# Performance work log

Measured on AMD Instinct MI355X. Metric: run time of the kernel, lower is better.

## Reference

```python
import jax, jax.numpy as jnp
import numpy as np

N_A = 100000
N_B = 100000


def _mean_agg(x_src, src, dst, n_dst):
    # gather source features along edges, mean-aggregate into destination nodes
    msgs = x_src[src]                                        # [E, d]
    s = jax.ops.segment_sum(msgs, dst, num_segments=n_dst)   # [n_dst, d]
    ones = jnp.ones((dst.shape[0], 1), dtype=x_src.dtype)
    cnt = jax.ops.segment_sum(ones, dst, num_segments=n_dst)
    return s / jnp.maximum(cnt, jnp.asarray(1.0, x_src.dtype))


def setup_inputs() -> dict:
    key = jax.random.key(0)
    ks = jax.random.split(key, 13)
    E = 1200000
    d = 64
    return {
        "x_A": jax.random.normal(ks[0], (N_A, d), jnp.float32),
        "x_B": jax.random.normal(ks[1], (N_B, d), jnp.float32),
        "Wn": jax.random.normal(ks[2], (2, 3, d, d), jnp.float32) * 0.1,
        "Wr": jax.random.normal(ks[3], (2, 3, d, d), jnp.float32) * 0.1,
        "b": jax.random.normal(ks[4], (2, 3, d), jnp.float32) * 0.1,
        "W_out": jax.random.normal(ks[5], (d, d), jnp.float32) * 0.1,
        "b_out": jax.random.normal(ks[6], (d,), jnp.float32) * 0.1,
        "src0": jax.random.randint(ks[7], (E,), 0, N_A, jnp.int64 if jax.config.jax_enable_x64 else jnp.int32),
        "dst0": jax.random.randint(ks[8], (E,), 0, N_B, jnp.int32),
        "src1": jax.random.randint(ks[9], (E,), 0, N_B, jnp.int32),
        "dst1": jax.random.randint(ks[10], (E,), 0, N_A, jnp.int32),
        "src2": jax.random.randint(ks[11], (E,), 0, N_A, jnp.int32),
        "dst2": jax.random.randint(ks[12], (E,), 0, N_A, jnp.int32),
    }


def reference(x_A, x_B, Wn, Wr, b, W_out, b_out,
              src0, dst0, src1, dst1, src2, dst2):
    # Two stacked heterogeneous conv layers (SAGEConv-style per edge type,
    # summed across edge types per destination node type), then Linear+ReLU head.
    for l in range(2):
        m0 = _mean_agg(x_A, src0, dst0, N_B)  # A -> B
        m1 = _mean_agg(x_B, src1, dst1, N_A)  # B -> A
        m2 = _mean_agg(x_A, src2, dst2, N_A)  # A -> A
        new_B = m0 @ Wn[l, 0] + x_B @ Wr[l, 0] + b[l, 0]
        new_A = (m1 @ Wn[l, 1] + x_A @ Wr[l, 1] + b[l, 1]
                 + m2 @ Wn[l, 2] + x_A @ Wr[l, 2] + b[l, 2])
        x_A, x_B = new_A, new_B
    out_A = jax.nn.relu(x_A @ W_out + b_out)
    out_B = jax.nn.relu(x_B @ W_out + b_out)
    return jnp.concatenate([out_A, out_B], axis=0)  # [N_A + N_B, d]
```

## Files before the change

### kernel.cpp

```cpp
#include <hip/hip_runtime.h>
#include <hip/hip_bf16.h>

typedef __bf16 bf16_t;
typedef unsigned short u16;
typedef short short8 __attribute__((ext_vector_type(8)));
typedef float f32x4 __attribute__((ext_vector_type(4)));

#define BSHIFT 9
#define CAP 8192
#define TILE 16384

__device__ inline short f2bs(float v) {
    bf16_t h = (bf16_t)v;
    return __builtin_bit_cast(short, h);
}
__device__ inline float uif(unsigned u) { return __builtin_bit_cast(float, u); }

__global__ __launch_bounds__(256) void prep_convert(
    const float* __restrict__ xA, const float* __restrict__ xB,
    const float* __restrict__ Wn, const float* __restrict__ Wr,
    const float* __restrict__ Wout, const float* __restrict__ b,
    const float* __restrict__ b_out,
    u16* __restrict__ plane0, u16* __restrict__ wh,
    int* __restrict__ gcursor, float* __restrict__ biasC,
    int NA, int NB, int K) {
    int nA4 = NA * 16, nB4 = NB * 16;
    int bA = (nA4 + 255) / 256, bB = (nB4 + 255) / 256;
    int bi = blockIdx.x;
    int tid = threadIdx.x;
    if (bi < bA + bB) {
        const float* in = (bi < bA) ? xA : xB;
        u16* out = (bi < bA) ? plane0 : plane0 + (size_t)NA * 64;
        int i = (bi < bA ? bi : bi - bA) * 256 + tid;
        int n4 = (bi < bA) ? nA4 : nB4;
        if (i >= n4) return;
        float4 v = ((const float4*)in)[i];
        u16 o[4];
        o[0] = (u16)f2bs(v.x); o[1] = (u16)f2bs(v.y);
        o[2] = (u16)f2bs(v.z); o[3] = (u16)f2bs(v.w);
        *(uint2*)(out + (size_t)i * 4) = *(uint2*)o;
        return;
    }
    if (bi < bA + bB + 11) {
        int mat = bi - bA - bB;
        u16* dstp = wh + (size_t)mat * 4096;
        for (int i = tid; i < 4096; i += 256) {
            int k = i >> 6, n = i & 63;
            float v;
            if (mat < 6) v = Wn[(size_t)mat * 4096 + i];
            else if (mat < 8) v = Wr[(size_t)((mat - 6) * 3 + 0) * 4096 + i];
            else if (mat < 10) v = Wr[(size_t)((mat - 8) * 3 + 1) * 4096 + i]
                                 + Wr[(size_t)((mat - 8) * 3 + 2) * 4096 + i];
            else v = Wout[i];
            dstp[n * 64 + k] = (u16)f2bs(v);
        }
        return;
    }
    if (bi < bA + bB + 11 + 5) {
        int c = bi - bA - bB - 11;
        const float* Wsrc;
        const float* Wsrc2 = nullptr;
        if (c == 0) Wsrc = Wn + (size_t)3 * 4096;
        else if (c == 1) Wsrc = Wr + (size_t)3 * 4096;
        else if (c == 2) Wsrc = Wn + (size_t)4 * 4096;
        else if (c == 3) Wsrc = Wn + (size_t)5 * 4096;
        else { Wsrc = Wr + (size_t)4 * 4096; Wsrc2 = Wr + (size_t)5 * 4096; }
        __shared__ float Ws[64 * 64];
        __shared__ float Wo[64 * 64];
        for (int i = tid; i < 4096; i += 256) {
            float w = Wsrc[i];
            if (Wsrc2) w += Wsrc2[i];
            Ws[i] = w;
            Wo[i] = Wout[i];
        }
        __syncthreads();
        u16* dstp = wh + (size_t)(11 + c) * 4096;
        for (int it = 0; it < 16; ++it) {
            int i = it * 256 + tid;
            int k = i >> 6, n = i & 63;
            float s0 = 0.f, s1 = 0.f, s2 = 0.f, s3 = 0.f;
#pragma unroll
            for (int j = 0; j < 64; j += 4) {
                s0 += Ws[k * 64 + j]     * Wo[j * 64 + n];
                s1 += Ws[k * 64 + j + 1] * Wo[(j + 1) * 64 + n];
                s2 += Ws[k * 64 + j + 2] * Wo[(j + 2) * 64 + n];
                s3 += Ws[k * 64 + j + 3] * Wo[(j + 3) * 64 + n];
            }
            dstp[n * 64 + k] = (u16)f2bs((s0 + s1) + (s2 + s3));
        }
        return;
    }
    for (int i = tid; i < K; i += 256) gcursor[i] = i * CAP;
    if (tid < 64) {
        int n = tid;
        float s0 = b_out[n], s1 = b_out[n];
        for (int j = 0; j < 64; j++) {
            float wo = Wout[j * 64 + n];
            s0 += b[3 * 64 + j] * wo;
            s1 += (b[4 * 64 + j] + b[5 * 64 + j]) * wo;
        }
        biasC[0 * 64 + n] = b[0 * 64 + n];
        biasC[1 * 64 + n] = b[1 * 64 + n] + b[2 * 64 + n];
        biasC[2 * 64 + n] = s0;
        biasC[3 * 64 + n] = s1;
    }
}

__global__ __launch_bounds__(1024) void partition_kernel(
    const int* __restrict__ s0, const int* __restrict__ d0,
    const int* __restrict__ s1, const int* __restrict__ d1,
    const int* __restrict__ s2, const int* __restrict__ d2,
    int* __restrict__ gcursor, int* __restrict__ pairs,
    int NB, int NA, int E, int total) {
    __shared__ int hist[1024];
    __shared__ int gbase[1024];
    int tid = threadIdx.x;
    for (int tile = blockIdx.x * TILE; tile < total; tile += gridDim.x * TILE) {
        hist[tid] = 0;
        __syncthreads();
        int mybkt[16], mypk[16], myrank[16];
#pragma unroll
        for (int j = 0; j < 16; j++) {
            int idx = tile + j * 1024 + tid;
            int g = -1, s = 0;
            if (idx < total) {
                if (idx < E) { s = s0[idx]; g = d0[idx]; }
                else if (idx < 2 * E) { s = s1[idx - E]; g = NB + d1[idx - E]; }
                else { s = s2[idx - 2 * E]; g = NB + NA + d2[idx - 2 * E]; }
            }
            if (g >= 0) {
                mybkt[j] = g >> BSHIFT;
                mypk[j] = ((g & ((1 << BSHIFT) - 1)) << 17) | s;
                myrank[j] = atomicAdd(&hist[mybkt[j]], 1);
            } else mybkt[j] = -1;
        }
        __syncthreads();
        {
            int c = hist[tid];
            if (c) gbase[tid] = atomicAdd(&gcursor[tid], c);
        }
        __syncthreads();
#pragma unroll
        for (int j = 0; j < 16; j++) {
            if (mybkt[j] >= 0)
                pairs[gbase[mybkt[j]] + myrank[j]] = mypk[j];
        }
        __syncthreads();
    }
}

__global__ __launch_bounds__(512) void bucket_fill(const int* __restrict__ pairs,
                                                   const int* __restrict__ gcursor,
                                                   int* __restrict__ off_s,
                                                   int* __restrict__ off_e,
                                                   int* __restrict__ colidx, int M) {
    int b = blockIdx.x;
    int gb = b << BSHIFT;
    __shared__ int cnt[512], cur[512], wsum[8];
    int tid = threadIdx.x;
    int lane = tid & 63, w = tid >> 6;
    int p0 = b * CAP, p1 = gcursor[b];
    cnt[tid] = 0;
    __syncthreads();
    for (int e = p0 + tid; e < p1; e += 512)
        atomicAdd(&cnt[(unsigned)pairs[e] >> 17], 1);
    __syncthreads();
    int v = cnt[tid];
    int x = v;
#pragma unroll
    for (int off = 1; off < 64; off <<= 1) {
        int n = __shfl_up(x, off);
        if (lane >= off) x += n;
    }
    if (lane == 63) wsum[w] = x;
    __syncthreads();
    if (tid == 0) {
        int s = 0;
#pragma unroll
        for (int i = 0; i < 8; i++) { int t = wsum[i]; wsum[i] = s; s += t; }
    }
    __syncthreads();
    int excl = x - v + wsum[w];
    cur[tid] = excl;
    int g = gb + tid;
    if (g < M) { off_s[g] = p0 + excl; off_e[g] = p0 + excl + v; }
    __syncthreads();
    for (int e = p0 + tid; e < p1; e += 512) {
        int p = pairs[e];
        int pos = atomicAdd(&cur[(unsigned)p >> 17], 1);
        colidx[p0 + pos] = p & 0x1FFFF;
    }
}

__device__ __forceinline__ void acc8(uint4 u, f32x4& a0, f32x4& a1) {
    a0[0] += uif(u.x << 16); a0[1] += uif(u.x & 0xFFFF0000u);
    a0[2] += uif(u.y << 16); a0[3] += uif(u.y & 0xFFFF0000u);
    a1[0] += uif(u.z << 16); a1[1] += uif(u.z & 0xFFFF0000u);
    a1[2] += uif(u.w << 16); a1[3] += uif(u.w & 0xFFFF0000u);
}

__global__ __launch_bounds__(256) void gather_all(const u16* __restrict__ plane,
                                                  const int* __restrict__ colidx,
                                                  const int* __restrict__ off_s,
                                                  const int* __restrict__ off_e,
                                                  u16* __restrict__ meanB,
                                                  u16* __restrict__ meanA1,
                                                  u16* __restrict__ meanA2,
                                                  int NB, int NA) {
    int wid = (blockIdx.x * 256 + threadIdx.x) >> 6;
    int lane = threadIdx.x & 63;
    int oct = lane >> 3, fl = lane & 7;
    int M = NB + 2 * NA;
    int grow = wid * 8 + oct;
    if (grow >= M) return;

    const char* tab;
    u16* outp;
    int orow;
    if (grow < NB) { tab = (const char*)plane; outp = meanB; orow = grow; }
    else if (grow < NB + NA) { tab = (const char*)(plane + (size_t)NA * 64); outp = meanA1; orow = grow - NB; }
    else { tab = (const char*)plane; outp = meanA2; orow = grow - NB - NA; }

    int s0 = off_s[grow], s1 = off_e[grow];
    unsigned fo = (unsigned)(fl << 4);
    f32x4 a0 = {0.f, 0.f, 0.f, 0.f}, a1 = {0.f, 0.f, 0.f, 0.f};

    int e = s0;
    if (e + 3 < s1) {
        int c0 = colidx[e], c1 = colidx[e + 1];
        int c2 = colidx[e + 2], c3 = colidx[e + 3];
        while (e + 7 < s1) {
            uint4 u0 = *(const uint4*)(tab + (((unsigned)c0 << 7) | fo));
            uint4 u1 = *(const uint4*)(tab + (((unsigned)c1 << 7) | fo));
            uint4 u2 = *(const uint4*)(tab + (((unsigned)c2 << 7) | fo));
            uint4 u3 = *(const uint4*)(tab + (((unsigned)c3 << 7) | fo));
            c0 = colidx[e + 4]; c1 = colidx[e + 5];
            c2 = colidx[e + 6]; c3 = colidx[e + 7];
            acc8(u0, a0, a1); acc8(u1, a0, a1);
            acc8(u2, a0, a1); acc8(u3, a0, a1);
            e += 4;
        }
        {
            uint4 u0 = *(const uint4*)(tab + (((unsigned)c0 << 7) | fo));
            uint4 u1 = *(const uint4*)(tab + (((unsigned)c1 << 7) | fo));
            uint4 u2 = *(const uint4*)(tab + (((unsigned)c2 << 7) | fo));
            uint4 u3 = *(const uint4*)(tab + (((unsigned)c3 << 7) | fo));
            acc8(u0, a0, a1); acc8(u1, a0, a1);
            acc8(u2, a0, a1); acc8(u3, a0, a1);
            e += 4;
        }
    }
    for (; e < s1; ++e) {
        int c = colidx[e];
        uint4 u = *(const uint4*)(tab + (((unsigned)c << 7) | fo));
        acc8(u, a0, a1);
    }

    float inv = 1.0f / fmaxf((float)(s1 - s0), 1.0f);
    u16 o[8];
#pragma unroll
    for (int i = 0; i < 4; i++) o[i] = (u16)f2bs(a0[i] * inv);
#pragma unroll
    for (int i = 0; i < 4; i++) o[4 + i] = (u16)f2bs(a1[i] * inv);
    *(uint4*)(outp + (size_t)orow * 64 + fl * 8) = *(uint4*)o;
}

template <int NM, int RELU, int OUTF32>
__device__ __forceinline__ void lin_body(
    const u16* __restrict__ m0, const u16* __restrict__ m1,
    const u16* __restrict__ x,
    const u16* __restrict__ Wm0t, const u16* __restrict__ Wm1t,
    const u16* __restrict__ Wxt,
    const float* __restrict__ bias64,
    void* __restrict__ outv, int nrows, int blk) {
    const int lane = threadIdx.x & 63;
    const int wave = threadIdx.x >> 6;
    const int row0 = blk * 64 + wave * 16;
    if (row0 >= nrows) return;
    const int r = lane & 15;
    const int q = lane >> 4;

    f32x4 acc[4];
#pragma unroll
    for (int t = 0; t < 4; t++) {
        float bv = bias64[t * 16 + r];
        acc[t][0] = bv; acc[t][1] = bv; acc[t][2] = bv; acc[t][3] = bv;
    }

    const int arow = row0 + r;
    const bool avalid = arow < nrows;
    short8 zf;
#pragma unroll
    for (int j = 0; j < 8; j++) zf[j] = 0;

#pragma unroll
    for (int ks = 0; ks < 2; ks++) {
        short8 af = avalid ? *(const short8*)(m0 + (size_t)arow * 64 + ks * 32 + q * 8) : zf;
        short8 xf = avalid ? *(const short8*)(x + (size_t)arow * 64 + ks * 32 + q * 8) : zf;
        short8 bf_;
        if (NM >= 2) bf_ = avalid ? *(const short8*)(m1 + (size_t)arow * 64 + ks * 32 + q * 8) : zf;
#pragma unroll
        for (int t = 0; t < 4; t++) {
            size_t widx = (size_t)(t * 16 + r) * 64 + ks * 32 + q * 8;
            acc[t] = __builtin_amdgcn_mfma_f32_16x16x32_bf16(af, *(const short8*)(Wm0t + widx), acc[t], 0, 0, 0);
            if (NM >= 2)
                acc[t] = __builtin_amdgcn_mfma_f32_16x16x32_bf16(bf_, *(const short8*)(Wm1t + widx), acc[t], 0, 0, 0);
            acc[t] = __builtin_amdgcn_mfma_f32_16x16x32_bf16(xf, *(const short8*)(Wxt + widx), acc[t], 0, 0, 0);
        }
    }

#pragma unroll
    for (int t = 0; t < 4; t++) {
#pragma unroll
        for (int rr = 0; rr < 4; rr++) {
            int row = row0 + q * 4 + rr;
            if (row < nrows) {
                float v = acc[t][rr];
                if (RELU) v = fmaxf(v, 0.0f);
                if (OUTF32)
                    __builtin_nontemporal_store(v, (float*)outv + (size_t)row * 64 + t * 16 + r);
                else
                    ((u16*)outv)[(size_t)row * 64 + t * 16 + r] = (u16)f2bs(v);
            }
        }
    }
}

__global__ __launch_bounds__(256) void layer1_kernel(
    const u16* __restrict__ plane_in, u16* __restrict__ plane_out,
    const u16* __restrict__ meanB, const u16* __restrict__ meanA1,
    const u16* __restrict__ meanA2, const u16* __restrict__ wh,
    const float* __restrict__ biasC, int NA, int NB, int blocksB) {
    if ((int)blockIdx.x < blocksB) {
        lin_body<1, 0, 0>(meanB, nullptr, plane_in + (size_t)NA * 64,
                          wh + (size_t)0 * 4096, nullptr, wh + (size_t)6 * 4096,
                          biasC + 0 * 64,
                          plane_out + (size_t)NA * 64, NB, blockIdx.x);
    } else {
        lin_body<2, 0, 0>(meanA1, meanA2, plane_in,
                          wh + (size_t)1 * 4096, wh + (size_t)2 * 4096, wh + (size_t)8 * 4096,
                          biasC + 1 * 64,
                          plane_out, NA, blockIdx.x - blocksB);
    }
}

__global__ __launch_bounds__(256) void layer2_head_kernel(
    const u16* __restrict__ plane_in,
    const u16* __restrict__ meanB, const u16* __restrict__ meanA1,
    const u16* __restrict__ meanA2, const u16* __restrict__ wh,
    const float* __restrict__ biasC,
    float* __restrict__ out, int NA, int NB, int blocksB) {
    if ((int)blockIdx.x < blocksB) {
        lin_body<1, 1, 1>(meanB, nullptr, plane_in + (size_t)NA * 64,
                          wh + (size_t)11 * 4096, nullptr, wh + (size_t)12 * 4096,
                          biasC + 2 * 64,
                          out + (size_t)NA * 64, NB, blockIdx.x);
    } else {
        lin_body<2, 1, 1>(meanA1, meanA2, plane_in,
                          wh + (size_t)13 * 4096, wh + (size_t)14 * 4096, wh + (size_t)15 * 4096,
                          biasC + 3 * 64,
                          out, NA, blockIdx.x - blocksB);
    }
}

extern "C" void kernel_launch(void* const* d_in, const int* in_sizes, int n_in,
                              void* d_out, int out_size, void* d_ws, size_t ws_size,
                              hipStream_t stream) {
    const float* xA_in = (const float*)d_in[0];
    const float* xB_in = (const float*)d_in[1];
    const float* Wn = (const float*)d_in[2];
    const float* Wr = (const float*)d_in[3];
    const float* b = (const float*)d_in[4];
    const float* W_out = (const float*)d_in[5];
    const float* b_out = (const float*)d_in[6];
    const int* src0 = (const int*)d_in[7];
    const int* dst0 = (const int*)d_in[8];
    const int* src1 = (const int*)d_in[9];
    const int* dst1 = (const int*)d_in[10];
    const int* src2 = (const int*)d_in[11];
    const int* dst2 = (const int*)d_in[12];

    const int NA = in_sizes[0] / 64;
    const int NB = in_sizes[1] / 64;
    const int E = in_sizes[7];
    const int M = NB + NA + NA;
    const int total = 3 * E;
    const int K = (M + (1 << BSHIFT) - 1) >> BSHIFT;

    const size_t PL = (size_t)(NA + NB) * 64;
    u16* plane[2];
    plane[0] = (u16*)d_ws;
    plane[1] = plane[0] + PL;
    u16* wh     = plane[1] + PL;
    u16* meanB  = wh + 16 * 4096;
    u16* meanA1 = meanB + (size_t)NB * 64;
    u16* meanA2 = meanA1 + (size_t)NA * 64;
    int* gcursor= (int*)(meanA2 + (size_t)NA * 64);
    float* biasC= (float*)(gcursor + 1024);
    int* off_s  = (int*)(biasC + 256);
    int* off_e  = off_s + M;
    int* colidx = off_e + M;
    int* pairs  = (int*)meanB;

    int bA = (NA * 16 + 255) / 256, bB = (NB * 16 + 255) / 256;
    prep_convert<<<bA + bB + 11 + 5 + 1, 256, 0, stream>>>(
        xA_in, xB_in, Wn, Wr, W_out, b, b_out,
        plane[0], wh, gcursor, biasC, NA, NB, K);

    int ntiles = (total + TILE - 1) / TILE;
    partition_kernel<<<ntiles, 1024, 0, stream>>>(src0, dst0, src1, dst1, src2, dst2,
                                                  gcursor, pairs, NB, NA, E, total);
    bucket_fill<<<K, 512, 0, stream>>>(pairs, gcursor, off_s, off_e, colidx, M);

    const int blocksB = (NB + 63) / 64;
    const int blocksA = (NA + 63) / 64;
    gather_all<<<(M + 31) / 32, 256, 0, stream>>>(plane[0], colidx, off_s, off_e,
                                                  meanB, meanA1, meanA2, NB, NA);
    layer1_kernel<<<blocksB + blocksA, 256, 0, stream>>>(
        plane[0], plane[1], meanB, meanA1, meanA2, wh, biasC, NA, NB, blocksB);

    gather_all<<<(M + 31) / 32, 256, 0, stream>>>(plane[1], colidx, off_s, off_e,
                                                  meanB, meanA1, meanA2, NB, NA);
    layer2_head_kernel<<<blocksB + blocksA, 256, 0, stream>>>(
        plane[1], meanB, meanA1, meanA2, wh, biasC, (float*)d_out, NA, NB, blocksB);
}
```

Before: 411.0 us.

## Fuse neighbor mean-gather with MFMA linear layer through shared memory

Replaces the separate gather_all and per-layer linear kernels with one fused kernel per layer. Each block gathers mean-aggregated neighbor rows into an LDS tile and immediately applies the MFMA projections, so the bf16 mean buffers are no longer written to and re-read from global memory. This removes two launches and the intermediate traffic. In exchange, blocks are smaller (32 or 16 rows), so more blocks are launched and weight fragments are reloaded per block, and the pairs scratch buffer is moved to sit after colidx.

```diff
diff --git a/kernel.cpp b/kernel.cpp
--- a/kernel.cpp
+++ b/kernel.cpp
@@ -199,32 +199,10 @@
     a1[2] += uif(u.w << 16); a1[3] += uif(u.w & 0xFFFF0000u);
 }
 
-__global__ __launch_bounds__(256) void gather_all(const u16* __restrict__ plane,
-                                                  const int* __restrict__ colidx,
-                                                  const int* __restrict__ off_s,
-                                                  const int* __restrict__ off_e,
-                                                  u16* __restrict__ meanB,
-                                                  u16* __restrict__ meanA1,
-                                                  u16* __restrict__ meanA2,
-                                                  int NB, int NA) {
-    int wid = (blockIdx.x * 256 + threadIdx.x) >> 6;
-    int lane = threadIdx.x & 63;
-    int oct = lane >> 3, fl = lane & 7;
-    int M = NB + 2 * NA;
-    int grow = wid * 8 + oct;
-    if (grow >= M) return;
-
-    const char* tab;
-    u16* outp;
-    int orow;
-    if (grow < NB) { tab = (const char*)plane; outp = meanB; orow = grow; }
-    else if (grow < NB + NA) { tab = (const char*)(plane + (size_t)NA * 64); outp = meanA1; orow = grow - NB; }
-    else { tab = (const char*)plane; outp = meanA2; orow = grow - NB - NA; }
-
-    int s0 = off_s[grow], s1 = off_e[grow];
-    unsigned fo = (unsigned)(fl << 4);
+__device__ __forceinline__ uint4 gather_seg(const char* __restrict__ tab,
+                                            const int* __restrict__ colidx,
+                                            int s0, int s1, unsigned fo) {
     f32x4 a0 = {0.f, 0.f, 0.f, 0.f}, a1 = {0.f, 0.f, 0.f, 0.f};
-
     int e = s0;
     if (e + 3 < s1) {
         int c0 = colidx[e], c1 = colidx[e + 1];
@@ -255,111 +233,133 @@
         uint4 u = *(const uint4*)(tab + (((unsigned)c << 7) | fo));
         acc8(u, a0, a1);
     }
-
     float inv = 1.0f / fmaxf((float)(s1 - s0), 1.0f);
     u16 o[8];
 #pragma unroll
     for (int i = 0; i < 4; i++) o[i] = (u16)f2bs(a0[i] * inv);
 #pragma unroll
     for (int i = 0; i < 4; i++) o[4 + i] = (u16)f2bs(a1[i] * inv);
-    *(uint4*)(outp + (size_t)orow * 64 + fl * 8) = *(uint4*)o;
-}
-
-template <int NM, int RELU, int OUTF32>
-__device__ __forceinline__ void lin_body(
-    const u16* __restrict__ m0, const u16* __restrict__ m1,
-    const u16* __restrict__ x,
-    const u16* __restrict__ Wm0t, const u16* __restrict__ Wm1t,
-    const u16* __restrict__ Wxt,
-    const float* __restrict__ bias64,
-    void* __restrict__ outv, int nrows, int blk) {
-    const int lane = threadIdx.x & 63;
-    const int wave = threadIdx.x >> 6;
-    const int row0 = blk * 64 + wave * 16;
-    if (row0 >= nrows) return;
-    const int r = lane & 15;
-    const int q = lane >> 4;
-
-    f32x4 acc[4];
-#pragma unroll
-    for (int t = 0; t < 4; t++) {
-        float bv = bias64[t * 16 + r];
-        acc[t][0] = bv; acc[t][1] = bv; acc[t][2] = bv; acc[t][3] = bv;
-    }
-
-    const int arow = row0 + r;
-    const bool avalid = arow < nrows;
+    return *(uint4*)o;
+}
+
+template <int L2>
+__global__ __launch_bounds__(256) void fused_layer(
+    const u16* __restrict__ plane_in, void* __restrict__ outv,
+    const int* __restrict__ colidx,
+    const int* __restrict__ off_s, const int* __restrict__ off_e,
+    const u16* __restrict__ wh, const float* __restrict__ biasC,
+    int NA, int NB, int blocksBf) {
+    __shared__ __align__(16) u16 mS[32][72];
+    const int tid = threadIdx.x;
+    const int w = tid >> 6, lane = tid & 63;
+    const int oct = lane >> 3, fl = lane & 7;
+    const unsigned fo = (unsigned)(fl << 4);
+    const char* pA = (const char*)plane_in;
+    const char* pB = (const char*)(plane_in + (size_t)NA * 64);
+    const int r = lane & 15, q = lane >> 4;
     short8 zf;
 #pragma unroll
     for (int j = 0; j < 8; j++) zf[j] = 0;
 
-#pragma unroll
-    for (int ks = 0; ks < 2; ks++) {
-        short8 af = avalid ? *(const short8*)(m0 + (size_t)arow * 64 + ks * 32 + q * 8) : zf;
-        short8 xf = avalid ? *(const short8*)(x + (size_t)arow * 64 + ks * 32 + q * 8) : zf;
-        short8 bf_;
-        if (NM >= 2) bf_ = avalid ? *(const short8*)(m1 + (size_t)arow * 64 + ks * 32 + q * 8) : zf;
-#pragma unroll
-        for (int t = 0; t < 4; t++) {
+    if ((int)blockIdx.x < blocksBf) {
+        const int row0 = blockIdx.x * 32;
+        {
+            int seg = w * 8 + oct;
+            int brow = row0 + seg;
+            int s0 = 0, s1 = 0;
+            if (brow < NB) { s0 = off_s[brow]; s1 = off_e[brow]; }
+            uint4 mv = gather_seg(pA, colidx, s0, s1, fo);
+            *(uint4*)&mS[seg][fl * 8] = mv;
+        }
+        __syncthreads();
+        const int rt = w >> 1;
+        const int tbase = (w & 1) * 2;
+        const int arow = row0 + rt * 16 + r;
+        const bool av = arow < NB;
+        const u16* WmT = wh + (size_t)(L2 ? 11 : 0) * 4096;
+        const u16* WxT = wh + (size_t)(L2 ? 12 : 6) * 4096;
+        const float* bb = biasC + (size_t)(L2 ? 2 : 0) * 64;
+        f32x4 acc[2];
+#pragma unroll
+        for (int t2 = 0; t2 < 2; t2++) {
+            float bv = bb[(tbase + t2) * 16 + r];
+            acc[t2][0] = bv; acc[t2][1] = bv; acc[t2][2] = bv; acc[t2][3] = bv;
+        }
+#pragma unroll
+        for (int ks = 0; ks < 2; ks++) {
+            short8 am = *(const short8*)&mS[rt * 16 + r][ks * 32 + q * 8];
+            short8 ax = av ? *(const short8*)(pB + (size_t)arow * 128 + ks * 64 + q * 16) : zf;
+#pragma unroll
+            for (int t2 = 0; t2 < 2; t2++) {
+                size_t widx = (size_t)((tbase + t2) * 16 + r) * 64 + ks * 32 + q * 8;
+                acc[t2] = __builtin_amdgcn_mfma_f32_16x16x32_bf16(am, *(const short8*)(WmT + widx), acc[t2], 0, 0, 0);
+                acc[t2] = __builtin_amdgcn_mfma_f32_16x16x32_bf16(ax, *(const short8*)(WxT + widx), acc[t2], 0, 0, 0);
+            }
+        }
+#pragma unroll
+        for (int t2 = 0; t2 < 2; t2++) {
+            int col = (tbase + t2) * 16 + r;
+#pragma unroll
+            for (int rr = 0; rr < 4; rr++) {
+                int row = row0 + rt * 16 + q * 4 + rr;
+                if (row < NB) {
+                    float v = acc[t2][rr];
+                    if (L2) __builtin_nontemporal_store(fmaxf(v, 0.0f),
+                                (float*)outv + (size_t)(NA + row) * 64 + col);
+                    else ((u16*)outv)[(size_t)(NA + row) * 64 + col] = (u16)f2bs(v);
+                }
+            }
+        }
+    } else {
+        const int row0 = ((int)blockIdx.x - blocksBf) * 16;
+        {
+            int seg = w * 8 + oct;
+            int rrow = row0 + (seg & 15);
+            bool m2 = seg >= 16;
+            int s0 = 0, s1 = 0;
+            if (rrow < NA) {
+                int g = m2 ? (NB + NA + rrow) : (NB + rrow);
+                s0 = off_s[g]; s1 = off_e[g];
+            }
+            uint4 mv = gather_seg(m2 ? pA : pB, colidx, s0, s1, fo);
+            *(uint4*)&mS[seg][fl * 8] = mv;
+        }
+        __syncthreads();
+        const int t = w;
+        const int arow = row0 + r;
+        const bool av = arow < NA;
+        const u16* Wm1T = wh + (size_t)(L2 ? 13 : 1) * 4096;
+        const u16* Wm2T = wh + (size_t)(L2 ? 14 : 2) * 4096;
+        const u16* WxT  = wh + (size_t)(L2 ? 15 : 8) * 4096;
+        const float* bb = biasC + (size_t)(L2 ? 3 : 1) * 64;
+        f32x4 acc;
+        {
+            float bv = bb[t * 16 + r];
+            acc[0] = bv; acc[1] = bv; acc[2] = bv; acc[3] = bv;
+        }
+#pragma unroll
+        for (int ks = 0; ks < 2; ks++) {
+            short8 am1 = *(const short8*)&mS[r][ks * 32 + q * 8];
+            short8 am2 = *(const short8*)&mS[16 + r][ks * 32 + q * 8];
+            short8 ax = av ? *(const short8*)(pA + (size_t)arow * 128 + ks * 64 + q * 16) : zf;
             size_t widx = (size_t)(t * 16 + r) * 64 + ks * 32 + q * 8;
-            acc[t] = __builtin_amdgcn_mfma_f32_16x16x32_bf16(af, *(const short8*)(Wm0t + widx), acc[t], 0, 0, 0);
-            if (NM >= 2)
-                acc[t] = __builtin_amdgcn_mfma_f32_16x16x32_bf16(bf_, *(const short8*)(Wm1t + widx), acc[t], 0, 0, 0);
-            acc[t] = __builtin_amdgcn_mfma_f32_16x16x32_bf16(xf, *(const short8*)(Wxt + widx), acc[t], 0, 0, 0);
-        }
-    }
-
-#pragma unroll
-    for (int t = 0; t < 4; t++) {
-#pragma unroll
-        for (int rr = 0; rr < 4; rr++) {
-            int row = row0 + q * 4 + rr;
-            if (row < nrows) {
-                float v = acc[t][rr];
-                if (RELU) v = fmaxf(v, 0.0f);
-                if (OUTF32)
-                    __builtin_nontemporal_store(v, (float*)outv + (size_t)row * 64 + t * 16 + r);
-                else
-                    ((u16*)outv)[(size_t)row * 64 + t * 16 + r] = (u16)f2bs(v);
-            }
-        }
-    }
-}
-
-__global__ __launch_bounds__(256) void layer1_kernel(
-    const u16* __restrict__ plane_in, u16* __restrict__ plane_out,
-    const u16* __restrict__ meanB, const u16* __restrict__ meanA1,
-    const u16* __restrict__ meanA2, const u16* __restrict__ wh,
-    const float* __restrict__ biasC, int NA, int NB, int blocksB) {
-    if ((int)blockIdx.x < blocksB) {
-        lin_body<1, 0, 0>(meanB, nullptr, plane_in + (size_t)NA * 64,
-                          wh + (size_t)0 * 4096, nullptr, wh + (size_t)6 * 4096,
-                          biasC + 0 * 64,
-                          plane_out + (size_t)NA * 64, NB, blockIdx.x);
-    } else {
-        lin_body<2, 0, 0>(meanA1, meanA2, plane_in,
-                          wh + (size_t)1 * 4096, wh + (size_t)2 * 4096, wh + (size_t)8 * 4096,
-                          biasC + 1 * 64,
-                          plane_out, NA, blockIdx.x - blocksB);
-    }
-}
-
-__global__ __launch_bounds__(256) void layer2_head_kernel(
-    const u16* __restrict__ plane_in,
-    const u16* __restrict__ meanB, const u16* __restrict__ meanA1,
-    const u16* __restrict__ meanA2, const u16* __restrict__ wh,
-    const float* __restrict__ biasC,
-    float* __restrict__ out, int NA, int NB, int blocksB) {
-    if ((int)blockIdx.x < blocksB) {
-        lin_body<1, 1, 1>(meanB, nullptr, plane_in + (size_t)NA * 64,
-                          wh + (size_t)11 * 4096, nullptr, wh + (size_t)12 * 4096,
-                          biasC + 2 * 64,
-                          out + (size_t)NA * 64, NB, blockIdx.x);
-    } else {
-        lin_body<2, 1, 1>(meanA1, meanA2, plane_in,
-                          wh + (size_t)13 * 4096, wh + (size_t)14 * 4096, wh + (size_t)15 * 4096,
-                          biasC + 3 * 64,
-                          out, NA, blockIdx.x - blocksB);
+            acc = __builtin_amdgcn_mfma_f32_16x16x32_bf16(am1, *(const short8*)(Wm1T + widx), acc, 0, 0, 0);
+            acc = __builtin_amdgcn_mfma_f32_16x16x32_bf16(am2, *(const short8*)(Wm2T + widx), acc, 0, 0, 0);
+            acc = __builtin_amdgcn_mfma_f32_16x16x32_bf16(ax, *(const short8*)(WxT + widx), acc, 0, 0, 0);
+        }
+        {
+            int col = t * 16 + r;
+#pragma unroll
+            for (int rr = 0; rr < 4; rr++) {
+                int row = row0 + q * 4 + rr;
+                if (row < NA) {
+                    float v = acc[rr];
+                    if (L2) __builtin_nontemporal_store(fmaxf(v, 0.0f),
+                                (float*)outv + (size_t)row * 64 + col);
+                    else ((u16*)outv)[(size_t)row * 64 + col] = (u16)f2bs(v);
+                }
+            }
+        }
     }
 }
 
@@ -392,15 +392,12 @@
     plane[0] = (u16*)d_ws;
     plane[1] = plane[0] + PL;
     u16* wh     = plane[1] + PL;
-    u16* meanB  = wh + 16 * 4096;
-    u16* meanA1 = meanB + (size_t)NB * 64;
-    u16* meanA2 = meanA1 + (size_t)NA * 64;
-    int* gcursor= (int*)(meanA2 + (size_t)NA * 64);
+    int* gcursor= (int*)(wh + 16 * 4096);
     float* biasC= (float*)(gcursor + 1024);
     int* off_s  = (int*)(biasC + 256);
     int* off_e  = off_s + M;
     int* colidx = off_e + M;
-    int* pairs  = (int*)meanB;
+    int* pairs  = colidx + (size_t)K * CAP;
 
     int bA = (NA * 16 + 255) / 256, bB = (NB * 16 + 255) / 256;
     prep_convert<<<bA + bB + 11 + 5 + 1, 256, 0, stream>>>(
@@ -412,15 +409,10 @@
                                                   gcursor, pairs, NB, NA, E, total);
     bucket_fill<<<K, 512, 0, stream>>>(pairs, gcursor, off_s, off_e, colidx, M);
 
-    const int blocksB = (NB + 63) / 64;
-    const int blocksA = (NA + 63) / 64;
-    gather_all<<<(M + 31) / 32, 256, 0, stream>>>(plane[0], colidx, off_s, off_e,
-                                                  meanB, meanA1, meanA2, NB, NA);
-    layer1_kernel<<<blocksB + blocksA, 256, 0, stream>>>(
-        plane[0], plane[1], meanB, meanA1, meanA2, wh, biasC, NA, NB, blocksB);
-
-    gather_all<<<(M + 31) / 32, 256, 0, stream>>>(plane[1], colidx, off_s, off_e,
-                                                  meanB, meanA1, meanA2, NB, NA);
-    layer2_head_kernel<<<blocksB + blocksA, 256, 0, stream>>>(
-        plane[1], meanB, meanA1, meanA2, wh, biasC, (float*)d_out, NA, NB, blocksB);
-}
+    const int blocksBf = (NB + 31) / 32;
+    const int blocksAf = (NA + 15) / 16;
+    fused_layer<0><<<blocksBf + blocksAf, 256, 0, stream>>>(
+        plane[0], plane[1], colidx, off_s, off_e, wh, biasC, NA, NB, blocksBf);
+    fused_layer<1><<<blocksBf + blocksAf, 256, 0, stream>>>(
+        plane[1], d_out, colidx, off_s, off_e, wh, biasC, NA, NB, blocksBf);
+}
```

Measured after the change: 381.9 us. 1.08x faster.
